# Kernel tuning notes

Measured on AMD Instinct MI355X. Metric: run time of the kernel, lower is better.

The kernel has to match this reference:

```python
import jax, jax.numpy as jnp
import numpy as np

N_NODES = 50000
N_EDGES = 800000
IN_DIM = 256
OUT_DIM = 32
HEADS = 4
NEG_SLOPE = 0.2  # PyG GATConv default
LN_EPS = 1e-5


def setup_inputs() -> dict:
    key = jax.random.key(0)
    ks = jax.random.split(key, 8)
    x = jax.random.normal(ks[0], (N_NODES, IN_DIM), dtype=jnp.float32)
    edge_index = jax.random.randint(ks[1], (2, N_EDGES), 0, N_NODES, dtype=jnp.int64)
    # Glorot-ish scaling for stability
    W = jax.random.normal(ks[2], (IN_DIM, HEADS * OUT_DIM), dtype=jnp.float32) / np.sqrt(IN_DIM)
    att_src = jax.random.normal(ks[3], (HEADS, OUT_DIM), dtype=jnp.float32) / np.sqrt(OUT_DIM)
    att_dst = jax.random.normal(ks[4], (HEADS, OUT_DIM), dtype=jnp.float32) / np.sqrt(OUT_DIM)
    bias = jax.random.normal(ks[5], (HEADS * OUT_DIM,), dtype=jnp.float32) * 0.02
    gamma = jnp.ones((HEADS * OUT_DIM,), dtype=jnp.float32)
    beta = jnp.zeros((HEADS * OUT_DIM,), dtype=jnp.float32)
    return {"x": x, "edge_index": edge_index, "W": W, "att_src": att_src,
            "att_dst": att_dst, "bias": bias, "gamma": gamma, "beta": beta}


def reference(x, edge_index, W, att_src, att_dst, bias, gamma, beta):
    N = x.shape[0]
    H, C = att_src.shape
    # --- GATConv (PyG semantics, eval mode so attention dropout is identity) ---
    # add self-loops (PyG default add_self_loops=True)
    loops = jnp.arange(N, dtype=edge_index.dtype)
    src = jnp.concatenate([edge_index[0], loops])  # [E+N]
    dst = jnp.concatenate([edge_index[1], loops])
    h = (x @ W).reshape(N, H, C)                    # [N,H,C] (lin has no bias)
    a_s = jnp.einsum('nhc,hc->nh', h, att_src)      # [N,H]
    a_d = jnp.einsum('nhc,hc->nh', h, att_dst)
    e = jax.nn.leaky_relu(a_s[src] + a_d[dst], NEG_SLOPE)  # [E+N,H]
    # segment softmax over incoming edges of each destination node
    emax = jax.ops.segment_max(e, dst, num_segments=N)     # every node has a self-loop
    ee = jnp.exp(e - emax[dst])
    denom = jax.ops.segment_sum(ee, dst, num_segments=N)
    alpha = ee / denom[dst]                                 # [E+N,H]
    msg = h[src] * alpha[:, :, None]                        # [E+N,H,C]
    out = jax.ops.segment_sum(msg, dst, num_segments=N).reshape(N, H * C) + bias
    # --- LayerNorm ---
    mu = out.mean(-1, keepdims=True)
    var = ((out - mu) ** 2).mean(-1, keepdims=True)
    out = (out - mu) * jax.lax.rsqrt(var + LN_EPS) * gamma + beta
    # --- dropout (eval: identity) + ELU ---
    return jax.nn.elu(out)
```

## Files before the change

kernel.cpp:

```cpp
#include <hip/hip_runtime.h>
#include <hip/hip_bf16.h>
#include <cstdint>
#include <cstddef>

#define N_NODES 50000
#define N_EDGES 800000
#define IN_DIM 256
#define HC 128
#define HEADS 4
#define NEG_SLOPE 0.2f
#define LN_EPS 1e-5f

#define POISON_I ((int)0xAAAAAAAAu)

#define NSB ((N_NODES + 255) / 256)

typedef _Float16 f16x8 __attribute__((ext_vector_type(8)));
typedef _Float16 f16x2 __attribute__((ext_vector_type(2)));
typedef float f32x4 __attribute__((ext_vector_type(4)));

__device__ __forceinline__ float lrelu(float x) { return x > 0.f ? x : NEG_SLOPE * x; }
__device__ __forceinline__ unsigned pack_h2(float a, float b) {
    f16x2 h; h[0] = (_Float16)a; h[1] = (_Float16)b;
    return *(unsigned*)&h;
}

__global__ __launch_bounds__(256) void k_histW(
    const int* __restrict__ ei, const float* __restrict__ W,
    _Float16* __restrict__ W16, int* __restrict__ counts,
    int* __restrict__ rank)
{
    int b = blockIdx.x;
    if (b < 16) {
        int c = b * 256 + threadIdx.x;
        int col = c & 15, quad = (c >> 4) & 3, nt = (c >> 6) & 7, kt = c >> 9;
        int n = nt * 16 + col;
        f16x8 v;
#pragma unroll
        for (int j = 0; j < 8; ++j) {
            int k = kt * 32 + quad * 8 + j;
            v[j] = (_Float16)W[k * HC + n];
        }
        *(f16x8*)(W16 + (size_t)c * 8) = v;
    } else {
        int e = (b - 16) * 256 + threadIdx.x;
        if (e < N_EDGES)
            rank[e] = atomicAdd(&counts[ei[N_EDGES + e]], 1) - POISON_I;
    }
}

__global__ __launch_bounds__(256) void k1_mfma(
    const float* __restrict__ x, const _Float16* __restrict__ W16,
    const float* __restrict__ att_src, const float* __restrict__ att_dst,
    _Float16* __restrict__ h16, float* __restrict__ a_s, float* __restrict__ a_d)
{
    __shared__ _Float16 Wlds[32768];
    const int tid = threadIdx.x;

    {
        const uint4* g4 = (const uint4*)W16;
        uint4* s4 = (uint4*)Wlds;
#pragma unroll
        for (int it = 0; it < 16; ++it) s4[it * 256 + tid] = g4[it * 256 + tid];
    }

    const int wave = tid >> 6;
    const int lane = tid & 63;
    const int col  = lane & 15;
    const int quad = lane >> 4;
    const int m0   = blockIdx.x * 64 + wave * 16;

    const int rowA = min(m0 + col, N_NODES - 1);
    const float* xrow = x + (size_t)rowA * IN_DIM + quad * 8;

    float4 xr[16];
#pragma unroll
    for (int kt = 0; kt < 8; ++kt) {
        xr[2 * kt]     = *(const float4*)(xrow + kt * 32);
        xr[2 * kt + 1] = *(const float4*)(xrow + kt * 32 + 4);
    }
    __syncthreads();

    f32x4 acc[8];
#pragma unroll
    for (int nt = 0; nt < 8; ++nt) acc[nt] = (f32x4){0.f, 0.f, 0.f, 0.f};

#pragma unroll
    for (int kt = 0; kt < 8; ++kt) {
        float4 xa = xr[2 * kt], xb = xr[2 * kt + 1];
        f16x8 a;
        a[0] = (_Float16)xa.x; a[1] = (_Float16)xa.y;
        a[2] = (_Float16)xa.z; a[3] = (_Float16)xa.w;
        a[4] = (_Float16)xb.x; a[5] = (_Float16)xb.y;
        a[6] = (_Float16)xb.z; a[7] = (_Float16)xb.w;
#pragma unroll
        for (int nt = 0; nt < 8; ++nt) {
            f16x8 b = *(const f16x8*)&Wlds[((kt * 8 + nt) * 64 + quad * 16 + col) * 8];
            acc[nt] = __builtin_amdgcn_mfma_f32_16x16x32_f16(a, b, acc[nt], 0, 0, 0);
        }
    }

    f16x2* h2g = (f16x2*)h16;
#pragma unroll
    for (int a2 = 0; a2 < 4; ++a2) {
#pragma unroll
        for (int r = 0; r < 4; ++r) {
            int row = m0 + quad * 4 + r;
            if (row < N_NODES) {
                f16x2 hv;
                hv[0] = (_Float16)acc[2 * a2][r];
                hv[1] = (_Float16)acc[2 * a2 + 1][r];
                h2g[(size_t)row * 64 + a2 * 16 + col] = hv;
            }
        }
    }

    float pS[4][4], pD[4][4];
#pragma unroll
    for (int hd = 0; hd < 4; ++hd)
#pragma unroll
        for (int r = 0; r < 4; ++r) { pS[hd][r] = 0.f; pD[hd][r] = 0.f; }

#pragma unroll
    for (int nt = 0; nt < 8; ++nt) {
        int ch = nt * 16 + col;
        float sv = att_src[ch], dv = att_dst[ch];
        int hd = nt >> 1;
#pragma unroll
        for (int r = 0; r < 4; ++r) {
            pS[hd][r] += acc[nt][r] * sv;
            pD[hd][r] += acc[nt][r] * dv;
        }
    }
#pragma unroll
    for (int off = 1; off < 16; off <<= 1) {
#pragma unroll
        for (int hd = 0; hd < 4; ++hd)
#pragma unroll
            for (int r = 0; r < 4; ++r) {
                pS[hd][r] += __shfl_xor(pS[hd][r], off, 16);
                pD[hd][r] += __shfl_xor(pD[hd][r], off, 16);
            }
    }
    if (col == 0) {
#pragma unroll
        for (int r = 0; r < 4; ++r) {
            int row = m0 + quad * 4 + r;
            if (row < N_NODES) {
#pragma unroll
                for (int hd = 0; hd < 4; ++hd) {
                    a_s[row * HEADS + hd] = pS[hd][r];
                    a_d[row * HEADS + hd] = pD[hd][r];
                }
            }
        }
    }
}

__global__ __launch_bounds__(256) void k_scan1(const int* __restrict__ counts,
                                               int* __restrict__ starts,
                                               int* __restrict__ bsum) {
    __shared__ int s[256];
    int i = blockIdx.x * 256 + threadIdx.x;
    int v = (i < N_NODES) ? (counts[i] - POISON_I) : 0;
    s[threadIdx.x] = v; __syncthreads();
#pragma unroll
    for (int off = 1; off < 256; off <<= 1) {
        int t = (threadIdx.x >= off) ? s[threadIdx.x - off] : 0;
        __syncthreads();
        s[threadIdx.x] += t;
        __syncthreads();
    }
    if (i < N_NODES) starts[i] = s[threadIdx.x] - v;
    if (threadIdx.x == 255) bsum[blockIdx.x] = s[255];
}
__global__ __launch_bounds__(256) void k_scan2(int* __restrict__ bsum, int nb) {
    __shared__ int s[256];
    int v = (threadIdx.x < nb) ? bsum[threadIdx.x] : 0;
    s[threadIdx.x] = v; __syncthreads();
#pragma unroll
    for (int off = 1; off < 256; off <<= 1) {
        int t = (threadIdx.x >= off) ? s[threadIdx.x - off] : 0;
        __syncthreads();
        s[threadIdx.x] += t;
        __syncthreads();
    }
    if (threadIdx.x < nb) bsum[threadIdx.x] = s[threadIdx.x] - v;
}

__global__ __launch_bounds__(256) void k_scatter(
    const int* __restrict__ ei, const int* __restrict__ starts,
    const int* __restrict__ bsum, const int* __restrict__ rank,
    const float* __restrict__ a_s, const float* __restrict__ a_d,
    int4* __restrict__ rec)
{
    int e = blockIdx.x * 256 + threadIdx.x;
    if (e >= N_EDGES) return;
    int src = ei[e], dst = ei[N_EDGES + e];
    float4 s4 = *(const float4*)(a_s + (size_t)src * HEADS);
    float4 d4 = *(const float4*)(a_d + (size_t)dst * HEADS);
    float w0 = __expf(lrelu(s4.x + d4.x));
    float w1 = __expf(lrelu(s4.y + d4.y));
    float w2 = __expf(lrelu(s4.z + d4.z));
    float w3 = __expf(lrelu(s4.w + d4.w));
    int p = starts[dst] + bsum[dst >> 8] + rank[e];
    int4 r;
    r.x = src;
    r.y = (int)pack_h2(w0, w1);
    r.z = (int)pack_h2(w2, w3);
    r.w = 0;
    rec[p] = r;
}

__global__ __launch_bounds__(256) void k_gather(
    const int* __restrict__ starts, const int* __restrict__ bsum,
    const int* __restrict__ counts, const int4* __restrict__ rec,
    const float* __restrict__ a_s, const float* __restrict__ a_d,
    const _Float16* __restrict__ h16, const float* __restrict__ bias,
    const float* __restrict__ gamma, const float* __restrict__ beta,
    float* __restrict__ out)
{
    __shared__ int   lsrc[256];
    __shared__ uint2 lw[256];

    int gid = blockIdx.x * 256 + threadIdx.x;
    int n = gid >> 6, lane = gid & 63;
    if (n >= N_NODES) return;

    const int wbase = (threadIdx.x >> 6) * 64;
    const int beg = starts[n] + bsum[n >> 8];
    const int deg = counts[n] - POISON_I;
    const int hd = lane >> 4;
    const f16x2* h2 = (const f16x2*)h16;
    const unsigned short* lwh = (const unsigned short*)&lw[wbase];

    const float wSelf = __expf(lrelu(a_s[n * HEADS + hd] + a_d[n * HEADS + hd]));
    float den = wSelf;
    f16x2 hv = h2[(size_t)n * 64 + lane];
    float acc0 = (float)hv[0] * wSelf;
    float acc1 = (float)hv[1] * wSelf;

    for (int base = 0; base < deg; base += 64) {
        int nc = min(64, deg - base);
        if (lane < nc) {
            int4 rv = rec[beg + base + lane];
            lsrc[wbase + lane] = rv.x;
            lw[wbase + lane] = (uint2){(unsigned)rv.y, (unsigned)rv.z};
        }
        int j = 0;
        for (; j + 8 <= nc; j += 8) {
            int s[8]; float w[8]; f16x2 hh[8];
#pragma unroll
            for (int k = 0; k < 8; ++k) {
                s[k] = lsrc[wbase + j + k];
                unsigned short uw = lwh[(j + k) * 4 + hd];
                _Float16 wf = *(_Float16*)&uw;
                w[k] = (float)wf;
            }
#pragma unroll
            for (int k = 0; k < 8; ++k) hh[k] = h2[(size_t)s[k] * 64 + lane];
#pragma unroll
            for (int k = 0; k < 8; ++k) {
                acc0 += (float)hh[k][0] * w[k];
                acc1 += (float)hh[k][1] * w[k];
                den  += w[k];
            }
        }
        for (; j < nc; ++j) {
            int s0 = lsrc[wbase + j];
            unsigned short uw = lwh[j * 4 + hd];
            _Float16 wf = *(_Float16*)&uw;
            float w0 = (float)wf;
            f16x2 hx = h2[(size_t)s0 * 64 + lane];
            acc0 += (float)hx[0] * w0;
            acc1 += (float)hx[1] * w0;
            den  += w0;
        }
    }

    const int c0 = (lane >> 4) * 32 + (lane & 15);
    const int c1 = c0 + 16;
    float v0 = acc0 / den + bias[c0];
    float v1 = acc1 / den + bias[c1];
    float s = v0 + v1;
#pragma unroll
    for (int off = 32; off; off >>= 1) s += __shfl_xor(s, off, 64);
    float mu = s * (1.f / 128.f);
    float d0 = v0 - mu, d1 = v1 - mu;
    float q = d0 * d0 + d1 * d1;
#pragma unroll
    for (int off = 32; off; off >>= 1) q += __shfl_xor(q, off, 64);
    float rs = rsqrtf(q * (1.f / 128.f) + LN_EPS);
    float o0 = d0 * rs * gamma[c0] + beta[c0];
    float o1 = d1 * rs * gamma[c1] + beta[c1];
    o0 = o0 > 0.f ? o0 : __expf(o0) - 1.f;
    o1 = o1 > 0.f ? o1 : __expf(o1) - 1.f;
    out[(size_t)n * HC + c0] = o0;
    out[(size_t)n * HC + c1] = o1;
}

extern "C" void kernel_launch(void* const* d_in, const int* in_sizes, int n_in,
                              void* d_out, int out_size, void* d_ws, size_t ws_size,
                              hipStream_t stream) {
    const float* x       = (const float*)d_in[0];
    const int*   ei      = (const int*)d_in[1];
    const float* W       = (const float*)d_in[2];
    const float* att_src = (const float*)d_in[3];
    const float* att_dst = (const float*)d_in[4];
    const float* bias    = (const float*)d_in[5];
    const float* gamma   = (const float*)d_in[6];
    const float* beta    = (const float*)d_in[7];
    float* out = (float*)d_out;

    char* ws = (char*)d_ws;
    _Float16* h16    = (_Float16*)(ws);
    float*    a_s    = (float*)(ws + 12800000);
    float*    a_d    = (float*)(ws + 13600000);
    int4*     rec    = (int4*) (ws + 14400000);
    int*      rank   = (int*)  (ws + 27200000);
    int*      counts = (int*)  (ws + 30400000);
    int*      starts = (int*)  (ws + 30600000);
    int*      bsum   = (int*)  (ws + 30800000);
    _Float16* W16    = (_Float16*)(ws + 30810240);

    k_histW<<<16 + (N_EDGES + 255) / 256, 256, 0, stream>>>(ei, W, W16, counts,
                                                            rank);
    k1_mfma<<<(N_NODES + 63) / 64, 256, 0, stream>>>(x, W16, att_src, att_dst,
                                                     h16, a_s, a_d);
    k_scan1<<<NSB, 256, 0, stream>>>(counts, starts, bsum);
    k_scan2<<<1, 256, 0, stream>>>(bsum, NSB);
    k_scatter<<<(N_EDGES + 255) / 256, 256, 0, stream>>>(ei, starts, bsum, rank,
                                                         a_s, a_d, rec);
    k_gather<<<(N_NODES * 64 + 255) / 256, 256, 0, stream>>>(
        starts, bsum, counts, rec, a_s, a_d, h16, bias, gamma, beta, out);
}
```

Baseline: 210.0 us.

## Fuse histogram and GEMM kernels; fold block-sum scan into consumers

The edge-degree histogram is merged into the MFMA projection kernel, with odd blocks doing atomics and even blocks doing the GEMM. Each GEMM block now converts and swizzles W from fp32 into LDS itself, so the separate W16 preprocessing pass is gone. The single-block scan2 launch is removed, and each scatter and gather block redundantly scans the 196 block sums in shared memory. Two launches are saved, paid for with redundant W conversion in every GEMM block and extra syncs and scan work in every scatter and gather block.

```diff
diff --git a/kernel.cpp b/kernel.cpp
--- a/kernel.cpp
+++ b/kernel.cpp
@@ -14,6 +14,8 @@
 #define POISON_I ((int)0xAAAAAAAAu)
 
 #define NSB ((N_NODES + 255) / 256)
+#define NGB ((N_NODES + 63) / 64)
+#define NHB 782
 
 typedef _Float16 f16x8 __attribute__((ext_vector_type(8)));
 typedef _Float16 f16x2 __attribute__((ext_vector_type(2)));
@@ -25,50 +27,34 @@
     return *(unsigned*)&h;
 }
 
-__global__ __launch_bounds__(256) void k_histW(
-    const int* __restrict__ ei, const float* __restrict__ W,
-    _Float16* __restrict__ W16, int* __restrict__ counts,
-    int* __restrict__ rank)
-{
-    int b = blockIdx.x;
-    if (b < 16) {
-        int c = b * 256 + threadIdx.x;
-        int col = c & 15, quad = (c >> 4) & 3, nt = (c >> 6) & 7, kt = c >> 9;
-        int n = nt * 16 + col;
-        f16x8 v;
-#pragma unroll
-        for (int j = 0; j < 8; ++j) {
-            int k = kt * 32 + quad * 8 + j;
-            v[j] = (_Float16)W[k * HC + n];
-        }
-        *(f16x8*)(W16 + (size_t)c * 8) = v;
-    } else {
-        int e = (b - 16) * 256 + threadIdx.x;
-        if (e < N_EDGES)
-            rank[e] = atomicAdd(&counts[ei[N_EDGES + e]], 1) - POISON_I;
-    }
-}
-
-__global__ __launch_bounds__(256) void k1_mfma(
-    const float* __restrict__ x, const _Float16* __restrict__ W16,
+__global__ __launch_bounds__(256) void k_fused(
+    const float* __restrict__ x, const float* __restrict__ W,
+    const int* __restrict__ ei,
     const float* __restrict__ att_src, const float* __restrict__ att_dst,
-    _Float16* __restrict__ h16, float* __restrict__ a_s, float* __restrict__ a_d)
+    _Float16* __restrict__ h16, float* __restrict__ a_s, float* __restrict__ a_d,
+    int* __restrict__ counts, int* __restrict__ rank)
 {
     __shared__ _Float16 Wlds[32768];
     const int tid = threadIdx.x;
-
-    {
-        const uint4* g4 = (const uint4*)W16;
-        uint4* s4 = (uint4*)Wlds;
-#pragma unroll
-        for (int it = 0; it < 16; ++it) s4[it * 256 + tid] = g4[it * 256 + tid];
-    }
-
+    const int b = blockIdx.x;
+
+    if (b & 1) {
+        const int eb = (b >> 1) << 10;
+#pragma unroll
+        for (int it = 0; it < 4; ++it) {
+            int e = eb + it * 256 + tid;
+            if (e < N_EDGES)
+                rank[e] = atomicAdd(&counts[ei[N_EDGES + e]], 1) - POISON_I;
+        }
+        return;
+    }
+
+    const int gb   = b >> 1;
     const int wave = tid >> 6;
     const int lane = tid & 63;
     const int col  = lane & 15;
     const int quad = lane >> 4;
-    const int m0   = blockIdx.x * 64 + wave * 16;
+    const int m0   = gb * 64 + wave * 16;
 
     const int rowA = min(m0 + col, N_NODES - 1);
     const float* xrow = x + (size_t)rowA * IN_DIM + quad * 8;
@@ -78,6 +64,19 @@
     for (int kt = 0; kt < 8; ++kt) {
         xr[2 * kt]     = *(const float4*)(xrow + kt * 32);
         xr[2 * kt + 1] = *(const float4*)(xrow + kt * 32 + 4);
+    }
+
+    {
+#pragma unroll
+        for (int it = 0; it < 16; ++it) {
+            int c = it * 256 + tid;
+            int ccol = c & 15, cquad = (c >> 4) & 3, cnt = (c >> 6) & 7, ckt = c >> 9;
+            const float* wp = W + (size_t)(ckt * 32 + cquad * 8) * HC + cnt * 16 + ccol;
+            f16x8 v;
+#pragma unroll
+            for (int j = 0; j < 8; ++j) v[j] = (_Float16)wp[j * HC];
+            *(f16x8*)(Wlds + (size_t)c * 8) = v;
+        }
     }
     __syncthreads();
 
@@ -95,8 +94,8 @@
         a[6] = (_Float16)xb.z; a[7] = (_Float16)xb.w;
 #pragma unroll
         for (int nt = 0; nt < 8; ++nt) {
-            f16x8 b = *(const f16x8*)&Wlds[((kt * 8 + nt) * 64 + quad * 16 + col) * 8];
-            acc[nt] = __builtin_amdgcn_mfma_f32_16x16x32_f16(a, b, acc[nt], 0, 0, 0);
+            f16x8 bb = *(const f16x8*)&Wlds[((kt * 8 + nt) * 64 + quad * 16 + col) * 8];
+            acc[nt] = __builtin_amdgcn_mfma_f32_16x16x32_f16(a, bb, acc[nt], 0, 0, 0);
         }
     }
 
@@ -174,18 +173,22 @@
     if (i < N_NODES) starts[i] = s[threadIdx.x] - v;
     if (threadIdx.x == 255) bsum[blockIdx.x] = s[255];
 }
-__global__ __launch_bounds__(256) void k_scan2(int* __restrict__ bsum, int nb) {
-    __shared__ int s[256];
-    int v = (threadIdx.x < nb) ? bsum[threadIdx.x] : 0;
-    s[threadIdx.x] = v; __syncthreads();
+
+__device__ __forceinline__ void scan_bsum(const int* __restrict__ bsum, int* sb) {
+    int t = threadIdx.x;
+    int v = (t < NSB) ? bsum[t] : 0;
+    sb[t] = v; __syncthreads();
 #pragma unroll
     for (int off = 1; off < 256; off <<= 1) {
-        int t = (threadIdx.x >= off) ? s[threadIdx.x - off] : 0;
+        int tv = (t >= off) ? sb[t - off] : 0;
         __syncthreads();
-        s[threadIdx.x] += t;
+        sb[t] += tv;
         __syncthreads();
     }
-    if (threadIdx.x < nb) bsum[threadIdx.x] = s[threadIdx.x] - v;
+    int ex = sb[t] - v;
+    __syncthreads();
+    sb[t] = ex;
+    __syncthreads();
 }
 
 __global__ __launch_bounds__(256) void k_scatter(
@@ -194,6 +197,9 @@
     const float* __restrict__ a_s, const float* __restrict__ a_d,
     int4* __restrict__ rec)
 {
+    __shared__ int sb[256];
+    scan_bsum(bsum, sb);
+
     int e = blockIdx.x * 256 + threadIdx.x;
     if (e >= N_EDGES) return;
     int src = ei[e], dst = ei[N_EDGES + e];
@@ -203,7 +209,7 @@
     float w1 = __expf(lrelu(s4.y + d4.y));
     float w2 = __expf(lrelu(s4.z + d4.z));
     float w3 = __expf(lrelu(s4.w + d4.w));
-    int p = starts[dst] + bsum[dst >> 8] + rank[e];
+    int p = starts[dst] + sb[dst >> 8] + rank[e];
     int4 r;
     r.x = src;
     r.y = (int)pack_h2(w0, w1);
@@ -222,13 +228,15 @@
 {
     __shared__ int   lsrc[256];
     __shared__ uint2 lw[256];
+    __shared__ int   sb[256];
+    scan_bsum(bsum, sb);
 
     int gid = blockIdx.x * 256 + threadIdx.x;
     int n = gid >> 6, lane = gid & 63;
     if (n >= N_NODES) return;
 
     const int wbase = (threadIdx.x >> 6) * 64;
-    const int beg = starts[n] + bsum[n >> 8];
+    const int beg = starts[n] + sb[n >> 8];
     const int deg = counts[n] - POISON_I;
     const int hd = lane >> 4;
     const f16x2* h2 = (const f16x2*)h16;
@@ -321,14 +329,10 @@
     int*      counts = (int*)  (ws + 30400000);
     int*      starts = (int*)  (ws + 30600000);
     int*      bsum   = (int*)  (ws + 30800000);
-    _Float16* W16    = (_Float16*)(ws + 30810240);
-
-    k_histW<<<16 + (N_EDGES + 255) / 256, 256, 0, stream>>>(ei, W, W16, counts,
-                                                            rank);
-    k1_mfma<<<(N_NODES + 63) / 64, 256, 0, stream>>>(x, W16, att_src, att_dst,
-                                                     h16, a_s, a_d);
+
+    k_fused<<<2 * NGB, 256, 0, stream>>>(x, W, ei, att_src, att_dst,
+                                         h16, a_s, a_d, counts, rank);
     k_scan1<<<NSB, 256, 0, stream>>>(counts, starts, bsum);
-    k_scan2<<<1, 256, 0, stream>>>(bsum, NSB);
     k_scatter<<<(N_EDGES + 255) / 256, 256, 0, stream>>>(ei, starts, bsum, rank,
                                                          a_s, a_d, rec);
     k_gather<<<(N_NODES * 64 + 255) / 256, 256, 0, stream>>>(
```

Result: faster. 204.8 us (-2.4%).
